# Optimization experiments

Hardware: AMD Instinct MI355X
Metric: run time of the kernel (lower is better)

## Reference

```python
import jax, jax.numpy as jnp
import numpy as np

B = 262144

def _init_linear(key, out_f, in_f):
    k1, k2 = jax.random.split(key)
    bound = 1.0 / np.sqrt(in_f)
    W = jax.random.uniform(k1, (out_f, in_f), jnp.float32, -bound, bound)
    b = jax.random.uniform(k2, (out_f,), jnp.float32, -bound, bound)
    return W, b

def setup_inputs() -> dict:
    key = jax.random.key(0)
    ks = jax.random.split(key, 7)
    x = jax.random.normal(ks[0], (B, 440), jnp.float32)
    bW1, bb1 = _init_linear(ks[1], 40, 40)
    bW2, bb2 = _init_linear(ks[2], 40, 40)
    bW3, bb3 = _init_linear(ks[3], 10, 40)
    sW1, sb1 = _init_linear(ks[4], 41, 41)
    sW2, sb2 = _init_linear(ks[5], 41, 41)
    sW3, sb3 = _init_linear(ks[6], 22, 41)
    return dict(x=x, bW1=bW1, bb1=bb1, bW2=bW2, bb2=bb2, bW3=bW3, bb3=bb3,
                sW1=sW1, sb1=sb1, sW2=sW2, sb2=sb2, sW3=sW3, sb3=sb3)

def reference(x, bW1, bb1, bW2, bb2, bW3, bb3, sW1, sb1, sW2, sb2, sW3, sb3):
    x_iabs = x[:, 0:40]                     # [B,40]
    x_ues = x[:, 40:].reshape(-1, 10, 40)   # [B,10,40] (one 40-dim block per segment)
    # big tower: Linear-ReLU-Linear-ReLU-Linear-Softmax
    h = jax.nn.relu(x_iabs @ bW1.T + bb1)
    h = jax.nn.relu(h @ bW2.T + bb2)
    iab = jax.nn.softmax(h @ bW3.T + bb3, axis=1)        # [B,10]
    # vectorized over the 10 segments: concat UE block with its IAB scalar
    small_in = jnp.concatenate([x_ues, iab[:, :, None]], axis=-1)  # [B,10,41]
    g = jax.nn.relu(jnp.einsum('bsi,oi->bso', small_in, sW1) + sb1)
    g = jax.nn.relu(jnp.einsum('bsi,oi->bso', g, sW2) + sb2)
    g = jax.nn.softmax(jnp.einsum('bsi,oi->bso', g, sW3) + sb3, axis=-1)  # [B,10,22]
    return g * iab[:, :, None]              # [B,10,22]
```

## Files before the change

kernel.cpp:

```cpp
#include <hip/hip_runtime.h>

typedef __attribute__((ext_vector_type(4))) float f32x4;
typedef __attribute__((ext_vector_type(8))) short s16x8;
typedef unsigned int u32;
typedef unsigned short ushort;

#define XDIM 440
#define ODIM 220
#define RPB  128
#define TPB  512
#define AW   52

__device__ __forceinline__ u32 cvtpk(float a, float b){
    u32 r; asm("v_cvt_pk_bf16_f32 %0, %1, %2" : "=v"(r) : "v"(a), "v"(b)); return r;
}
__device__ __forceinline__ void split8pk(const float* v, s16x8& h, s16x8& l){
    uint4 hu, lu; u32* hp=(u32*)&hu; u32* lp=(u32*)&lu;
    #pragma unroll
    for (int j=0;j<4;++j){
        u32 hk = cvtpk(v[2*j], v[2*j+1]);
        float h0 = __builtin_bit_cast(float, hk<<16);
        float h1 = __builtin_bit_cast(float, hk & 0xFFFF0000u);
        lp[j] = cvtpk(v[2*j]-h0, v[2*j+1]-h1);
        hp[j] = hk;
    }
    h = __builtin_bit_cast(s16x8,hu); l = __builtin_bit_cast(s16x8,lu);
}
__device__ __forceinline__ void ldsplit(const float* p, s16x8& h, s16x8& l){
    float a[8];
    *(float4*)(a)   = *(const float4*)(p);
    *(float4*)(a+4) = *(const float4*)(p+4);
    split8pk(a,h,l);
}
__device__ __forceinline__ s16x8 ld8u(const ushort* p){ return *(const s16x8*)p; }

__device__ __forceinline__ f32x4 mm3(s16x8 ah, s16x8 al, s16x8 bh, s16x8 bl, f32x4 c){
    c = __builtin_amdgcn_mfma_f32_16x16x32_bf16(ah, bh, c, 0, 0, 0);
    c = __builtin_amdgcn_mfma_f32_16x16x32_bf16(ah, bl, c, 0, 0, 0);
    c = __builtin_amdgcn_mfma_f32_16x16x32_bf16(al, bh, c, 0, 0, 0);
    return c;
}

__device__ __forceinline__ ushort bf_rne(float f){
    unsigned u = __builtin_bit_cast(unsigned, f);
    return (ushort)((u + 0x7FFFu + ((u >> 16) & 1u)) >> 16);
}

__global__ void prep_w(const float* __restrict__ bW1, const float* __restrict__ bW2,
                       const float* __restrict__ bW3, const float* __restrict__ sW1,
                       const float* __restrict__ sW2, const float* __restrict__ sW3,
                       const float* __restrict__ bb1, const float* __restrict__ bb2,
                       const float* __restrict__ bb3, const float* __restrict__ sb1,
                       const float* __restrict__ sb2, const float* __restrict__ sb3,
                       ushort* __restrict__ WH, ushort* __restrict__ WL,
                       float* __restrict__ BIAS, ushort* __restrict__ WF)
{
    int i = blockIdx.x * 256 + threadIdx.x;
    if (i < 15360) {
        int n = i >> 6, k = i & 63;
        float w = 0.f;
        if      (n < 48)  { int r = n;     if (r < 40 && k < 40) w = bW1[r*40+k]; }
        else if (n < 96)  { int r = n-48;  if (r < 40 && k < 40) w = bW2[r*40+k]; }
        else if (n < 112) { int r = n-96;  if (r < 10 && k < 40) w = bW3[r*40+k]; }
        else if (n < 160) { int r = n-112; if (r < 41 && k < 41) w = sW1[r*41+k]; }
        else if (n < 208) { int r = n-160; if (r < 41 && k < 41) w = sW2[r*41+k]; }
        else              { int r = n-208; if (r < 22 && k < 41) w = sW3[r*41+k]; }
        ushort h = bf_rne(w);
        float hf = __builtin_bit_cast(float, ((unsigned)h) << 16);
        WH[i] = h; WL[i] = bf_rne(w - hf);
    } else if (i < 15600) {
        int n = i - 15360;
        float b;
        if      (n < 48)  b = (n     < 40) ? bb1[n]     : 0.f;
        else if (n < 96)  b = (n-48  < 40) ? bb2[n-48]  : 0.f;
        else if (n < 112) b = (n-96  < 10) ? bb3[n-96]  : -1e30f;
        else if (n < 160) b = (n-112 < 41) ? sb1[n-112] : 0.f;
        else if (n < 208) b = (n-160 < 41) ? sb2[n-160] : 0.f;
        else              b = (n-208 < 22) ? sb3[n-208] : -1e30f;
        BIAS[n] = b;
    } else if (i < 23792) {
        int e = i - 15600;
        int fragid = e >> 9, rem = e & 511;
        int lane = rem >> 3, j = rem & 7;
        int t2 = fragid >> 1, hf2 = fragid & 1;
        int li = lane & 15, qq = lane >> 4;
        int r = t2*16 + li;
        int k = qq*8 + j;
        float w = 0.f;
        if      (r < 48) { if (r < 41)           w = sW1[r*41+k]; }
        else if (r < 96) { int rr=r-48; if (rr<41) w = sW2[rr*41+k]; }
        else             { int rr=r-96; if (rr<22) w = sW3[rr*41+k]; }
        ushort h = bf_rne(w);
        ushort v = h;
        if (hf2){ float hfv = __builtin_bit_cast(float, ((unsigned)h)<<16); v = bf_rne(w - hfv); }
        WF[e] = v;
    } else if (i < 28280) {
        int e = i - 23792;
        int lane = e / 136, c = e % 136;
        ushort v = 0;
        if (lane < 32 && c < 128){
            int fragid = c >> 3, j = c & 7;
            int t2 = fragid >> 1, hf2 = fragid & 1;
            int li = lane & 15, qq = (lane >> 4) & 1;
            int r = t2*16 + li;
            int k = 32 + qq*8 + j;
            float w = 0.f;
            if      (r < 48) { if (r<41 && k<41)            w = sW1[r*41+k]; }
            else if (r < 96) { int rr=r-48; if (rr<41 && k<41) w = sW2[rr*41+k]; }
            else             { int rr=r-96; if (rr<22 && k<41) w = sW3[rr*41+k]; }
            ushort h = bf_rne(w);
            v = h;
            if (hf2){ float hfv = __builtin_bit_cast(float, ((unsigned)h)<<16); v = bf_rne(w - hfv); }
        }
        WF[8192 + e] = v;
    }
}

__global__ __launch_bounds__(TPB, 4) void ran8(
    const float* __restrict__ x,
    const ushort* __restrict__ WH, const ushort* __restrict__ WL,
    const float* __restrict__ BIASg, const ushort* __restrict__ WFg,
    float* __restrict__ out, int nrow)
{
    __shared__ ushort Wlds[12680];
    __shared__ float  Act[RPB][AW];
    __shared__ float  guard[16];
    __shared__ float  biasS[240];

    const int tid = threadIdx.x;
    const int l   = tid & 63;
    const int w   = tid >> 6;
    const int q   = l >> 4;
    const int li  = l & 15;
    const int w16 = w * 16;
    const int R0  = blockIdx.x * RPB;
    const int arow = w16 + li;
    const int growC = min(R0 + arow, nrow - 1);
    const int wb1 = 8192 + ((l < 32) ? l*136 : 4352);

    {
        const u32* src = (const u32*)WFg;
        u32* dst = (u32*)Wlds;
        for (int i = tid; i < 6340; i += TPB) dst[i] = src[i];
    }
    for (int i = tid; i < 240; i += TPB) biasS[i] = BIASg[i];
    for (int i = tid; i < RPB*AW; i += TPB) ((float*)Act)[i] = 0.f;
    if (tid < 16) guard[tid] = 0.f;
    __syncthreads();

#define WF0(t2,hf) (*(const s16x8*)&Wlds[((t2)*2+(hf))*512 + l*8])
#define WF1(t2,hf) (*(const s16x8*)&Wlds[wb1 + ((t2)*2+(hf))*8])

    float pm[4];

    {
        const float* xp = x + (size_t)growC * XDIM;
        float a0[8], a1[8];
        *(float4*)(a0)   = *(const float4*)(xp + q*8);
        *(float4*)(a0+4) = *(const float4*)(xp + q*8 + 4);
        if (q == 0){
            *(float4*)(a1)   = *(const float4*)(xp + 32);
            *(float4*)(a1+4) = *(const float4*)(xp + 36);
        } else {
            #pragma unroll
            for (int j=0;j<8;++j) a1[j] = 0.f;
        }
        s16x8 ah0,al0,ah1,al1;
        split8pk(a0, ah0, al0); split8pk(a1, ah1, al1);
        #pragma unroll
        for (int nt=0; nt<3; ++nt){
            int n = nt*16 + li; float b = biasS[n];
            f32x4 acc = {b,b,b,b};
            acc = mm3(ah0,al0, ld8u(WH+n*64+q*8),    ld8u(WL+n*64+q*8),    acc);
            acc = mm3(ah1,al1, ld8u(WH+n*64+32+q*8), ld8u(WL+n*64+32+q*8), acc);
            #pragma unroll
            for (int r=0;r<4;++r)
                Act[w16+q*4+r][nt*16+li] = fmaxf(acc[r],0.f);
        }
    }
    {
        s16x8 ah0,al0,ah1,al1;
        ldsplit(&Act[arow][q*8],    ah0, al0);
        ldsplit(&Act[arow][32+q*8], ah1, al1);
        #pragma unroll
        for (int nt=0; nt<3; ++nt){
            int n = 48+nt*16+li; float b = biasS[n];
            f32x4 acc = {b,b,b,b};
            acc = mm3(ah0,al0, ld8u(WH+n*64+q*8),    ld8u(WL+n*64+q*8),    acc);
            acc = mm3(ah1,al1, ld8u(WH+n*64+32+q*8), ld8u(WL+n*64+32+q*8), acc);
            #pragma unroll
            for (int r=0;r<4;++r)
                Act[w16+q*4+r][nt*16+li] = fmaxf(acc[r],0.f);
        }
    }
    {
        s16x8 ah0,al0,ah1,al1;
        ldsplit(&Act[arow][q*8],    ah0, al0);
        ldsplit(&Act[arow][32+q*8], ah1, al1);
        int n = 96+li; float b = biasS[n];
        f32x4 acc = {b,b,b,b};
        acc = mm3(ah0,al0, ld8u(WH+n*64+q*8),    ld8u(WL+n*64+q*8),    acc);
        acc = mm3(ah1,al1, ld8u(WH+n*64+32+q*8), ld8u(WL+n*64+32+q*8), acc);
        #pragma unroll
        for (int r=0;r<4;++r){
            float v = acc[r];
            float m = v;
            m = fmaxf(m, __shfl_xor(m,1)); m = fmaxf(m, __shfl_xor(m,2));
            m = fmaxf(m, __shfl_xor(m,4)); m = fmaxf(m, __shfl_xor(m,8));
            float e = __expf(v - m);
            float sum = e;
            sum += __shfl_xor(sum,1); sum += __shfl_xor(sum,2);
            sum += __shfl_xor(sum,4); sum += __shfl_xor(sum,8);
            pm[r] = __fdividef(e, sum);
        }
    }

    const float* xrow = x + (size_t)growC * XDIM + 40;
    auto stage_load = [&](int S, float* pf0, float* pf1){
        const float* xp = xrow + S*40;
        *(float4*)(pf0)   = *(const float4*)(xp + q*8);
        *(float4*)(pf0+4) = *(const float4*)(xp + q*8 + 4);
        if (q == 0){
            *(float4*)(pf1)   = *(const float4*)(xp + 32);
            *(float4*)(pf1+4) = *(const float4*)(xp + 36);
        }
    };

    auto compute_slot = [&](int s, const float* pf0, const float* pf1){
        s16x8 ah0,al0,ah1,al1;
        int srcl = ((li & 12) << 2) + s;
        float t0 = __shfl(pm[0], srcl);
        float t1 = __shfl(pm[1], srcl);
        float t2 = __shfl(pm[2], srcl);
        float t3 = __shfl(pm[3], srcl);
        float iv = (li & 2) ? ((li & 1) ? t3 : t2) : ((li & 1) ? t1 : t0);
        split8pk(pf0, ah0, al0);
        float a1v[8];
        #pragma unroll
        for (int j=0;j<8;++j) a1v[j] = (q==0) ? pf1[j] : 0.f;
        if (q == 1) a1v[0] = iv;
        split8pk(a1v, ah1, al1);
        #pragma unroll
        for (int nt=0; nt<3; ++nt){
            float b = biasS[112+nt*16+li];
            f32x4 acc = {b,b,b,b};
            acc = mm3(ah0,al0, WF0(nt,0), WF0(nt,1), acc);
            acc = mm3(ah1,al1, WF1(nt,0), WF1(nt,1), acc);
            #pragma unroll
            for (int r=0;r<4;++r)
                Act[w16+q*4+r][nt*16+li] = fmaxf(acc[r],0.f);
        }
        ldsplit(&Act[arow][q*8],    ah0, al0);
        ldsplit(&Act[arow][32+q*8], ah1, al1);
        #pragma unroll
        for (int nt=0; nt<3; ++nt){
            float b = biasS[160+nt*16+li];
            f32x4 acc = {b,b,b,b};
            acc = mm3(ah0,al0, WF0(3+nt,0), WF0(3+nt,1), acc);
            acc = mm3(ah1,al1, WF1(3+nt,0), WF1(3+nt,1), acc);
            #pragma unroll
            for (int r=0;r<4;++r)
                Act[w16+q*4+r][nt*16+li] = fmaxf(acc[r],0.f);
        }
        ldsplit(&Act[arow][q*8],    ah0, al0);
        ldsplit(&Act[arow][32+q*8], ah1, al1);
        float b6 = biasS[208+li], b7 = biasS[224+li];
        f32x4 a6 = {b6,b6,b6,b6}, a7 = {b7,b7,b7,b7};
        a6 = mm3(ah0,al0, WF0(6,0), WF0(6,1), a6);
        a6 = mm3(ah1,al1, WF1(6,0), WF1(6,1), a6);
        a7 = mm3(ah0,al0, WF0(7,0), WF0(7,1), a7);
        a7 = mm3(ah1,al1, WF1(7,0), WF1(7,1), a7);
        #pragma unroll
        for (int r=0;r<4;++r){
            float v0 = a6[r], v1 = a7[r];
            float m = fmaxf(v0, v1);
            m = fmaxf(m, __shfl_xor(m,1)); m = fmaxf(m, __shfl_xor(m,2));
            m = fmaxf(m, __shfl_xor(m,4)); m = fmaxf(m, __shfl_xor(m,8));
            float e0 = __expf(v0 - m), e1 = __expf(v1 - m);
            float sum = e0 + e1;
            sum += __shfl_xor(sum,1); sum += __shfl_xor(sum,2);
            sum += __shfl_xor(sum,4); sum += __shfl_xor(sum,8);
            float ivr = __shfl(pm[r], (l & 48) + s);
            float sc = __fdividef(ivr, sum);
            int lr = w16 + q*4 + r;
            Act[lr][li] = e0 * sc;
            if (li < 6) Act[lr][16 + li] = e1 * sc;
        }
        #pragma unroll
        for (int it = 0; it < 3; ++it){
            int i = l + 64*it;
            if (i < 176){
                int lr = i/11, pc = i - lr*11;
                if (R0 + w16 + lr < nrow)
                    *(float2*)(out + (size_t)(R0+w16+lr)*ODIM + s*22 + pc*2)
                        = *(const float2*)&Act[w16+lr][pc*2];
            }
        }
    };

    float pfA0[8], pfA1[8], pfB0[8], pfB1[8];
    stage_load(0, pfA0, pfA1);
    #pragma unroll 1
    for (int s = 0; s < 10; s += 2){
        stage_load(s+1, pfB0, pfB1);
        compute_slot(s, pfA0, pfA1);
        if (s+2 < 10) stage_load(s+2, pfA0, pfA1);
        compute_slot(s+1, pfB0, pfB1);
    }
#undef WF0
#undef WF1
    (void)guard;
}

extern "C" void kernel_launch(void* const* d_in, const int* in_sizes, int n_in,
                              void* d_out, int out_size, void* d_ws, size_t ws_size,
                              hipStream_t stream)
{
    (void)n_in; (void)out_size; (void)ws_size;
    const float* x   = (const float*)d_in[0];
    const float* bW1 = (const float*)d_in[1];
    const float* bb1 = (const float*)d_in[2];
    const float* bW2 = (const float*)d_in[3];
    const float* bb2 = (const float*)d_in[4];
    const float* bW3 = (const float*)d_in[5];
    const float* bb3 = (const float*)d_in[6];
    const float* sW1 = (const float*)d_in[7];
    const float* sb1 = (const float*)d_in[8];
    const float* sW2 = (const float*)d_in[9];
    const float* sb2 = (const float*)d_in[10];
    const float* sW3 = (const float*)d_in[11];
    const float* sb3 = (const float*)d_in[12];
    float* outp = (float*)d_out;

    ushort* WH  = (ushort*)d_ws;
    ushort* WL  = WH + 15360;
    float*  BIAS= (float*)((char*)d_ws + 61440);
    ushort* WF  = (ushort*)((char*)d_ws + 62464);

    const int rows = in_sizes[0] / XDIM;

    prep_w<<<111, 256, 0, stream>>>(bW1, bW2, bW3, sW1, sW2, sW3,
                                    bb1, bb2, bb3, sb1, sb2, sb3,
                                    WH, WL, BIAS, WF);

    const int grid = (rows + RPB - 1) / RPB;
    ran8<<<grid, TPB, 0, stream>>>(x, WH, WL, BIAS, WF, outp, rows);
}
```

Baseline: 294.3 us.

## Replace double-buffered prefetch with single buffer and raise occupancy target

Collapses the two-slot register double buffer into one buffer whose next-segment load is issued after the current inputs are split to bf16, before the matmuls. Raises the launch-bounds waves-per-EU hint from 4 to 6 and drops restrict on x and out. The aim is lower register pressure and more resident waves to hide memory latency. In exchange there is less prefetch distance, shared-memory use may cap occupancy anyway, and the tighter register target risks spills.

```diff
diff --git a/kernel.cpp b/kernel.cpp
--- a/kernel.cpp
+++ b/kernel.cpp
@@ -116,11 +116,11 @@
     }
 }
 
-__global__ __launch_bounds__(TPB, 4) void ran8(
-    const float* __restrict__ x,
+__global__ __launch_bounds__(TPB, 6) void ran9(
+    const float* x,
     const ushort* __restrict__ WH, const ushort* __restrict__ WL,
     const float* __restrict__ BIASg, const ushort* __restrict__ WFg,
-    float* __restrict__ out, int nrow)
+    float* out, int nrow)
 {
     __shared__ ushort Wlds[12680];
     __shared__ float  Act[RPB][AW];
@@ -216,17 +216,21 @@
     }
 
     const float* xrow = x + (size_t)growC * XDIM + 40;
-    auto stage_load = [&](int S, float* pf0, float* pf1){
-        const float* xp = xrow + S*40;
+    float pf0[8], pf1[8];
+    #pragma unroll
+    for (int j=0;j<8;++j) pf1[j] = 0.f;
+    {
+        const float* xp = xrow;
         *(float4*)(pf0)   = *(const float4*)(xp + q*8);
         *(float4*)(pf0+4) = *(const float4*)(xp + q*8 + 4);
         if (q == 0){
             *(float4*)(pf1)   = *(const float4*)(xp + 32);
             *(float4*)(pf1+4) = *(const float4*)(xp + 36);
         }
-    };
-
-    auto compute_slot = [&](int s, const float* pf0, const float* pf1){
+    }
+
+    #pragma unroll 1
+    for (int s = 0; s < 10; ++s){
         s16x8 ah0,al0,ah1,al1;
         int srcl = ((li & 12) << 2) + s;
         float t0 = __shfl(pm[0], srcl);
@@ -237,9 +241,18 @@
         split8pk(pf0, ah0, al0);
         float a1v[8];
         #pragma unroll
-        for (int j=0;j<8;++j) a1v[j] = (q==0) ? pf1[j] : 0.f;
+        for (int j=0;j<8;++j) a1v[j] = pf1[j];
         if (q == 1) a1v[0] = iv;
         split8pk(a1v, ah1, al1);
+        if (s < 9){
+            const float* xp = xrow + (s+1)*40;
+            *(float4*)(pf0)   = *(const float4*)(xp + q*8);
+            *(float4*)(pf0+4) = *(const float4*)(xp + q*8 + 4);
+            if (q == 0){
+                *(float4*)(pf1)   = *(const float4*)(xp + 32);
+                *(float4*)(pf1+4) = *(const float4*)(xp + 36);
+            }
+        }
         #pragma unroll
         for (int nt=0; nt<3; ++nt){
             float b = biasS[112+nt*16+li];
@@ -296,16 +309,6 @@
                         = *(const float2*)&Act[w16+lr][pc*2];
             }
         }
-    };
-
-    float pfA0[8], pfA1[8], pfB0[8], pfB1[8];
-    stage_load(0, pfA0, pfA1);
-    #pragma unroll 1
-    for (int s = 0; s < 10; s += 2){
-        stage_load(s+1, pfB0, pfB1);
-        compute_slot(s, pfA0, pfA1);
-        if (s+2 < 10) stage_load(s+2, pfA0, pfA1);
-        compute_slot(s+1, pfB0, pfB1);
     }
 #undef WF0
 #undef WF1
@@ -344,5 +347,5 @@
                                     WH, WL, BIAS, WF);
 
     const int grid = (rows + RPB - 1) / RPB;
-    ran8<<<grid, TPB, 0, stream>>>(x, WH, WL, BIAS, WF, outp, rows);
-}
+    ran9<<<grid, TPB, 0, stream>>>(x, WH, WL, BIAS, WF, outp, rows);
+}
```

Result: slower. 329.4 us (+11.9%).
